# Kernel tuning notes

Hardware: AMD Instinct MI355X
Metric: run time of the kernel (lower is better)

## Reference

```python
import jax, jax.numpy as jnp
import numpy as np

NUM_HEADS = 32
HIDDEN = 4096
ROPE_HID = 2048            # per-head rope dim = 64
Q_LOW = 1536
KV_LOW = 512
B, S = 1, 2048


def _rope(x):
    """Rotate-half RoPE over the last dim of x: [B, S, D]."""
    D = x.shape[-1]
    seq = x.shape[1]
    inv_freq = 1.0 / (10000.0 ** (jnp.arange(0, D, 2, dtype=jnp.float32) / D))  # [D/2]
    ang = jnp.arange(seq, dtype=jnp.float32)[:, None] * inv_freq[None, :]       # [S, D/2]
    cos, sin = jnp.cos(ang), jnp.sin(ang)
    x1, x2 = x[..., : D // 2], x[..., D // 2 :]
    return jnp.concatenate([x1 * cos - x2 * sin, x2 * cos + x1 * sin], axis=-1).astype(x.dtype)


def _rms_norm(x):
    # torch F.rms_norm with no weight; eps defaults to machine epsilon of dtype
    eps = jnp.finfo(x.dtype).eps
    return x * jax.lax.rsqrt(jnp.mean(x * x, axis=-1, keepdims=True) + eps)


def _lin(x, W, b):
    return x @ W.T + b


def setup_inputs() -> dict:
    key = jax.random.key(0)
    ks = jax.random.split(key, 12)
    s = 0.02
    inp = {
        "hidden_state": jax.random.normal(ks[0], (B, S, HIDDEN), jnp.float32),
        "attention_mask": jnp.zeros((B, S, S), jnp.float32),
        "Wq_lr": jax.random.normal(ks[1], (Q_LOW, HIDDEN), jnp.float32) * s,
        "bq_lr": jnp.zeros((Q_LOW,), jnp.float32),
        "Wq_rope": jax.random.normal(ks[2], (ROPE_HID, Q_LOW), jnp.float32) * s,
        "bq_rope": jnp.zeros((ROPE_HID,), jnp.float32),
        "Wq_c": jax.random.normal(ks[3], (HIDDEN, Q_LOW), jnp.float32) * s,
        "bq_c": jnp.zeros((HIDDEN,), jnp.float32),
        "Wkv": jax.random.normal(ks[4], (KV_LOW, HIDDEN), jnp.float32) * s,
        "bkv": jnp.zeros((KV_LOW,), jnp.float32),
        "Wk_rope": jax.random.normal(ks[5], (ROPE_HID // NUM_HEADS, HIDDEN), jnp.float32) * s,
        "bk_rope": jnp.zeros((ROPE_HID // NUM_HEADS,), jnp.float32),
        "Wk_c": jax.random.normal(ks[6], (HIDDEN, KV_LOW), jnp.float32) * s,
        "bk_c": jnp.zeros((HIDDEN,), jnp.float32),
        "Wv": jax.random.normal(ks[7], (HIDDEN, KV_LOW), jnp.float32) * s,
        "bv": jnp.zeros((HIDDEN,), jnp.float32),
        "Wo": jax.random.normal(ks[8], (HIDDEN, HIDDEN), jnp.float32) * s,
        "bo": jnp.zeros((HIDDEN,), jnp.float32),
    }
    return inp


def reference(hidden_state, attention_mask, Wq_lr, bq_lr, Wq_rope, bq_rope, Wq_c, bq_c,
              Wkv, bkv, Wk_rope, bk_rope, Wk_c, bk_c, Wv, bv, Wo, bo):
    H = NUM_HEADS
    b, s, _ = hidden_state.shape
    hd_c = HIDDEN // H        # 128 content head dim
    hd_r = ROPE_HID // H      # 64 rope head dim

    # ---- queries ----
    c_q = _lin(hidden_state, Wq_lr, bq_lr)                       # [B,S,Qlow]
    q_content = _lin(c_q, Wq_c, bq_c).reshape(b, s, H, hd_c)     # [B,S,H,128]
    q_rope = _rope(_lin(c_q, Wq_rope, bq_rope))                  # rope over full 2048 dim
    q_rope = q_rope.reshape(b, s, H, hd_r)                       # [B,S,H,64]
    q = jnp.concatenate([q_content, q_rope], axis=-1)            # [B,S,H,192]

    # ---- keys / values ----
    c_kv = _lin(hidden_state, Wkv, bkv)                          # [B,S,KVlow]
    k_content = _lin(c_kv, Wk_c, bk_c).reshape(b, s, H, hd_c)    # [B,S,H,128]
    k_rope = _rope(_lin(hidden_state, Wk_rope, bk_rope))         # [B,S,64] shared across heads
    k_rope = jnp.broadcast_to(k_rope[:, :, None, :], (b, s, H, hd_r))
    k = jnp.concatenate([k_content, k_rope], axis=-1)            # [B,S,H,192]
    v = _lin(c_kv, Wv, bv).reshape(b, s, H, hd_c)                # [B,S,H,128]

    # ---- qk rms norm (enable_qk_norm=True) ----
    q = _rms_norm(q)
    k = _rms_norm(k)

    # ---- sdpa (bmm + scale + mask + softmax + bmm) ----
    scale = 1.0 / jnp.sqrt(jnp.asarray(q.shape[-1], q.dtype))
    scores = jnp.einsum('bqhd,bkhd->bhqk', q, k) * scale         # [B,H,S,S]
    scores = scores + attention_mask[:, None, :, :]
    attn = jax.nn.softmax(scores, axis=-1)
    out = jnp.einsum('bhqk,bkhd->bqhd', attn, v)                 # [B,S,H,128]
    out = out.reshape(b, s, HIDDEN)
    return _lin(out, Wo, bo)
```

## Files before the change

kernel.cpp:

```cpp
#include <hip/hip_runtime.h>
#include <hip/hip_bf16.h>
#include <math.h>


#define S_LEN 2048
#define HID 4096
#define NH 32
#define HD_C 128
#define HD 192
#define QSTRIDE (NH * HD)

typedef __bf16 bf16x8 __attribute__((ext_vector_type(8)));
typedef float f32x4 __attribute__((ext_vector_type(4)));

__device__ __forceinline__ unsigned short f2bu(float x) {
  __hip_bfloat16 h = __float2bfloat16(x);
  return *reinterpret_cast<unsigned short*>(&h);
}

__global__ __launch_bounds__(256) void f32_to_bf16_vec(
    const float* __restrict__ src, unsigned short* __restrict__ dst, int n8) {
  for (int i = blockIdx.x * 256 + threadIdx.x; i < n8; i += gridDim.x * 256) {
    const float4 a = ((const float4*)src)[(size_t)i * 2];
    const float4 b = ((const float4*)src)[(size_t)i * 2 + 1];
    unsigned short u[8] = {f2bu(a.x), f2bu(a.y), f2bu(a.z), f2bu(a.w),
                           f2bu(b.x), f2bu(b.y), f2bu(b.z), f2bu(b.w)};
    *(float4*)&dst[(size_t)i * 8] = *(float4*)u;
  }
}

__global__ __launch_bounds__(256) void gemm_bf16(
    const unsigned short* __restrict__ A, const unsigned short* __restrict__ W,
    const float* __restrict__ bias, void* __restrict__ Cv,
    int M, int N, int K, int out_mode, int bias_mode) {
  __shared__ __align__(16) unsigned short As[128 * 32];
  __shared__ __align__(16) unsigned short Bs[128 * 32];

  const int tid = threadIdx.x;
  const int wid = tid >> 6, lane = tid & 63;
  const int cl = lane & 15, g = lane >> 4;
  const int wr = wid >> 1, wc = wid & 1;
  const int m0 = blockIdx.y * 128, n0 = blockIdx.x * 128;

  f32x4 acc[4][4] = {};

  for (int k0 = 0; k0 < K; k0 += 32) {
    __syncthreads();
#pragma unroll
    for (int j = 0; j < 2; ++j) {
      const int c = j * 256 + wid * 64 + lane;
      const unsigned short* ga =
          &A[(size_t)(m0 + (c >> 2)) * K + k0 + (c & 3) * 8];
      __builtin_amdgcn_global_load_lds(
          (const __attribute__((address_space(1))) unsigned int*)ga,
          (__attribute__((address_space(3))) unsigned int*)&As[(size_t)(j * 256 + wid * 64) * 8],
          16, 0, 0);
      const unsigned short* gb =
          &W[(size_t)(n0 + (c >> 2)) * K + k0 + (c & 3) * 8];
      __builtin_amdgcn_global_load_lds(
          (const __attribute__((address_space(1))) unsigned int*)gb,
          (__attribute__((address_space(3))) unsigned int*)&Bs[(size_t)(j * 256 + wid * 64) * 8],
          16, 0, 0);
    }
    __syncthreads();

    bf16x8 a[4], b[4];
#pragma unroll
    for (int m = 0; m < 4; ++m)
      a[m] = *(const bf16x8*)&As[(size_t)(wr * 64 + m * 16 + cl) * 32 + g * 8];
#pragma unroll
    for (int n = 0; n < 4; ++n)
      b[n] = *(const bf16x8*)&Bs[(size_t)(wc * 64 + n * 16 + cl) * 32 + g * 8];
#pragma unroll
    for (int m = 0; m < 4; ++m)
#pragma unroll
      for (int n = 0; n < 4; ++n)
        acc[m][n] =
            __builtin_amdgcn_mfma_f32_16x16x32_bf16(a[m], b[n], acc[m][n], 0, 0, 0);
  }

#pragma unroll
  for (int m = 0; m < 4; ++m) {
    const int row = m0 + wr * 64 + m * 16 + g * 4;
#pragma unroll
    for (int n = 0; n < 4; ++n) {
      const int col = n0 + wc * 64 + n * 16 + cl;
#pragma unroll
      for (int r = 0; r < 4; ++r) {
        const float val =
            acc[m][n][r] + (bias_mode ? bias[row + r] : bias[col]);
        if (out_mode == 0)
          ((float*)Cv)[(size_t)(row + r) * N + col] = val;
        else if (out_mode == 1)
          ((__hip_bfloat16*)Cv)[(size_t)(row + r) * QSTRIDE + (col >> 7) * HD +
                                (col & 127)] = __float2bfloat16(val);
        else
          ((__hip_bfloat16*)Cv)[(size_t)(row + r) * N + col] =
              __float2bfloat16(val);
      }
    }
  }
}

template <int TM>
__global__ __launch_bounds__(256) void gemm_bt(
    const float* __restrict__ A, const float* __restrict__ W,
    const float* __restrict__ bias, void* __restrict__ Cv,
    int M, int N, int K, int out_mode) {
  constexpr int RPT = TM / 16;
  __shared__ float As[16][TM + 4];
  __shared__ float Ws[16][68];

  const int tid = threadIdx.x;
  const int tx = tid & 15, ty = tid >> 4;
  const int m0 = blockIdx.y * TM, n0 = blockIdx.x * 64;

  float acc[RPT][4];
#pragma unroll
  for (int i = 0; i < RPT; ++i)
#pragma unroll
    for (int j = 0; j < 4; ++j) acc[i][j] = 0.f;

  for (int k0 = 0; k0 < K; k0 += 16) {
    if (tid < TM * 4) {
      const int r = tid >> 2, c4 = (tid & 3) * 4;
      float4 av = *(const float4*)&A[(size_t)(m0 + r) * K + k0 + c4];
      As[c4 + 0][r] = av.x; As[c4 + 1][r] = av.y;
      As[c4 + 2][r] = av.z; As[c4 + 3][r] = av.w;
    }
    {
      const int r = tid >> 2, c4 = (tid & 3) * 4;
      float4 wv = *(const float4*)&W[(size_t)(n0 + r) * K + k0 + c4];
      Ws[c4 + 0][r] = wv.x; Ws[c4 + 1][r] = wv.y;
      Ws[c4 + 2][r] = wv.z; Ws[c4 + 3][r] = wv.w;
    }
    __syncthreads();
#pragma unroll
    for (int kk = 0; kk < 16; ++kk) {
      const float4 wv = *(const float4*)&Ws[kk][tx * 4];
      const float a = As[kk][ty];
      acc[0][0] += a * wv.x; acc[0][1] += a * wv.y;
      acc[0][2] += a * wv.z; acc[0][3] += a * wv.w;
    }
    __syncthreads();
  }

#pragma unroll
  for (int i = 0; i < RPT; ++i) {
    const int m = m0 + ty * RPT + i;
#pragma unroll
    for (int j = 0; j < 4; ++j) {
      const int n = n0 + tx * 4 + j;
      ((float*)Cv)[(size_t)m * N + n] = acc[i][j] + bias[n];
    }
  }
}

__global__ __launch_bounds__(256) void rope_scatter_q(
    const float* __restrict__ pre, __hip_bfloat16* __restrict__ qh) {
  const int i = blockIdx.x * blockDim.x + threadIdx.x;
  if (i >= S_LEN * 1024) return;
  const int s = i >> 10, p = i & 1023;
  const double invf = pow(10000.0, -((double)(2 * p) / 2048.0));
  double sd, cd;
  sincos((double)s * invf, &sd, &cd);
  const float c = (float)cd, sn = (float)sd;
  const float x1 = pre[(size_t)s * 2048 + p];
  const float x2 = pre[(size_t)s * 2048 + p + 1024];
  const int g1 = p, g2 = p + 1024;
  qh[(size_t)s * QSTRIDE + (g1 >> 6) * HD + 128 + (g1 & 63)] =
      __float2bfloat16(x1 * c - x2 * sn);
  qh[(size_t)s * QSTRIDE + (g2 >> 6) * HD + 128 + (g2 & 63)] =
      __float2bfloat16(x2 * c + x1 * sn);
}

__global__ __launch_bounds__(64) void rope_bcast_k(
    const float* __restrict__ pre, __hip_bfloat16* __restrict__ kh) {
  const int s = blockIdx.x;
  const int j = threadIdx.x;
  const float x = pre[s * 64 + j];
  const float partner = pre[s * 64 + (j ^ 32)];
  const int p = j & 31;
  const double invf = pow(10000.0, -((double)(2 * p) / 64.0));
  double sd, cd;
  sincos((double)s * invf, &sd, &cd);
  const float val = (j < 32) ? x * (float)cd - partner * (float)sd
                             : x * (float)cd + partner * (float)sd;
  const __hip_bfloat16 hv = __float2bfloat16(val);
  for (int h = 0; h < NH; ++h)
    kh[(size_t)s * QSTRIDE + h * HD + 128 + j] = hv;
}

__global__ __launch_bounds__(256) void rmsnorm_rows_bf16(
    __hip_bfloat16* __restrict__ X, int nrows, float scale) {
  const int row = blockIdx.x * 4 + (threadIdx.x >> 6);
  const int lane = threadIdx.x & 63;
  if (row >= nrows) return;
  __hip_bfloat16* p = X + (size_t)row * HD;
  const float v0 = __bfloat162float(p[lane]);
  const float v1 = __bfloat162float(p[lane + 64]);
  const float v2 = __bfloat162float(p[lane + 128]);
  float ss = v0 * v0 + v1 * v1 + v2 * v2;
#pragma unroll
  for (int off = 32; off > 0; off >>= 1) ss += __shfl_xor(ss, off, 64);
  const float r = scale / sqrtf(ss * (1.0f / 192.0f) + 1.1920929e-7f);
  p[lane] = __float2bfloat16(v0 * r);
  p[lane + 64] = __float2bfloat16(v1 * r);
  p[lane + 128] = __float2bfloat16(v2 * r);
}

__global__ __launch_bounds__(256, 2) void flash_attn_mfma2(
    const __hip_bfloat16* __restrict__ Qh, const __hip_bfloat16* __restrict__ Kh,
    const __hip_bfloat16* __restrict__ Vtg, const float* __restrict__ mask,
    __hip_bfloat16* __restrict__ O) {
  __shared__ __align__(16) unsigned short Ks[64][200];
  __shared__ __align__(16) unsigned short Vs[128][72];
  __shared__ __align__(16) unsigned short Ps[4][32][72];

  const int tid = threadIdx.x;
  const int wid = tid >> 6, lane = tid & 63;
  const int cl = lane & 15, g = lane >> 4;
  const int h = blockIdx.y;
  const int Q0 = blockIdx.x * 128 + wid * 32;

  const unsigned short* Q = (const unsigned short*)Qh;
  const unsigned short* K = (const unsigned short*)Kh;
  const unsigned short* Vt = (const unsigned short*)Vtg;

  bf16x8 qreg[2][6];
#pragma unroll
  for (int qt = 0; qt < 2; ++qt)
#pragma unroll
    for (int c = 0; c < 6; ++c)
      qreg[qt][c] = *(const bf16x8*)&Q[(size_t)(Q0 + qt * 16 + cl) * QSTRIDE +
                                       h * HD + c * 32 + g * 8];

  float mprev[2] = {-INFINITY, -INFINITY};
  float lsum[2] = {0.f, 0.f};
  f32x4 acc[2][8] = {};

  for (int k0 = 0; k0 < S_LEN; k0 += 64) {
    __syncthreads();
#pragma unroll
    for (int i = 0; i < 6; ++i) {
      const int c = tid + i * 256;
      const int r = c / 24, cc = c % 24;
      *(float4*)&Ks[r][cc * 8] =
          *(const float4*)&K[(size_t)(k0 + r) * QSTRIDE + h * HD + cc * 8];
    }
#pragma unroll
    for (int i = 0; i < 4; ++i) {
      const int c = tid + i * 256;
      const int d = c >> 3, jc = c & 7;
      *(float4*)&Vs[d][jc * 8] =
          *(const float4*)&Vt[(size_t)(h * HD_C + d) * S_LEN + k0 + jc * 8];
    }
    __syncthreads();

    f32x4 s[2][4] = {};
#pragma unroll
    for (int t = 0; t < 4; ++t) {
#pragma unroll
      for (int c = 0; c < 6; ++c) {
        const bf16x8 kf = *(const bf16x8*)&Ks[t * 16 + cl][c * 32 + g * 8];
        s[0][t] = __builtin_amdgcn_mfma_f32_16x16x32_bf16(kf, qreg[0][c],
                                                          s[0][t], 0, 0, 0);
        s[1][t] = __builtin_amdgcn_mfma_f32_16x16x32_bf16(kf, qreg[1][c],
                                                          s[1][t], 0, 0, 0);
      }
    }
#pragma unroll
    for (int qt = 0; qt < 2; ++qt)
#pragma unroll
      for (int t = 0; t < 4; ++t) {
        const float4 mk = *(const float4*)&mask[(size_t)(Q0 + qt * 16 + cl) *
                                                    S_LEN +
                                                k0 + t * 16 + g * 4];
        s[qt][t][0] += mk.x; s[qt][t][1] += mk.y;
        s[qt][t][2] += mk.z; s[qt][t][3] += mk.w;
      }

#pragma unroll
    for (int qt = 0; qt < 2; ++qt) {
      float mloc = s[qt][0][0];
#pragma unroll
      for (int t = 0; t < 4; ++t)
#pragma unroll
        for (int r = 0; r < 4; ++r) mloc = fmaxf(mloc, s[qt][t][r]);
      mloc = fmaxf(mloc, __shfl_xor(mloc, 16, 64));
      mloc = fmaxf(mloc, __shfl_xor(mloc, 32, 64));
      const float mnew = fmaxf(mprev[qt], mloc);
      const float rsc = __expf(mprev[qt] - mnew);
      mprev[qt] = mnew;
      float p[4][4];
      float ll = 0.f;
#pragma unroll
      for (int t = 0; t < 4; ++t)
#pragma unroll
        for (int r = 0; r < 4; ++r) {
          p[t][r] = __expf(s[qt][t][r] - mnew);
          ll += p[t][r];
        }
      ll += __shfl_xor(ll, 16, 64);
      ll += __shfl_xor(ll, 32, 64);
      lsum[qt] = lsum[qt] * rsc + ll;
#pragma unroll
      for (int dt = 0; dt < 8; ++dt) {
        acc[qt][dt][0] *= rsc; acc[qt][dt][1] *= rsc;
        acc[qt][dt][2] *= rsc; acc[qt][dt][3] *= rsc;
      }
#pragma unroll
      for (int t = 0; t < 4; ++t) {
        unsigned short u[4] = {f2bu(p[t][0]), f2bu(p[t][1]), f2bu(p[t][2]),
                               f2bu(p[t][3])};
        *(double*)&Ps[wid][qt * 16 + cl][t * 16 + g * 4] = *(double*)u;
      }
    }

#pragma unroll
    for (int c = 0; c < 2; ++c) {
      const bf16x8 pf0 = *(const bf16x8*)&Ps[wid][cl][c * 32 + g * 8];
      const bf16x8 pf1 = *(const bf16x8*)&Ps[wid][16 + cl][c * 32 + g * 8];
#pragma unroll
      for (int dt = 0; dt < 8; ++dt) {
        const bf16x8 vf = *(const bf16x8*)&Vs[dt * 16 + cl][c * 32 + g * 8];
        acc[0][dt] = __builtin_amdgcn_mfma_f32_16x16x32_bf16(vf, pf0,
                                                             acc[0][dt], 0, 0, 0);
        acc[1][dt] = __builtin_amdgcn_mfma_f32_16x16x32_bf16(vf, pf1,
                                                             acc[1][dt], 0, 0, 0);
      }
    }
  }

#pragma unroll
  for (int qt = 0; qt < 2; ++qt) {
    const float il = 1.0f / lsum[qt];
    const size_t base = (size_t)(Q0 + qt * 16 + cl) * HID + h * HD_C;
#pragma unroll
    for (int dt = 0; dt < 8; ++dt) {
      unsigned short u[4] = {
          f2bu(acc[qt][dt][0] * il), f2bu(acc[qt][dt][1] * il),
          f2bu(acc[qt][dt][2] * il), f2bu(acc[qt][dt][3] * il)};
      *(double*)&((unsigned short*)O)[base + dt * 16 + g * 4] = *(double*)u;
    }
  }
}

extern "C" void kernel_launch(void* const* d_in, const int* in_sizes, int n_in,
                              void* d_out, int out_size, void* d_ws,
                              size_t ws_size, hipStream_t stream) {
  const float* X       = (const float*)d_in[0];
  const float* mask    = (const float*)d_in[1];
  const float* Wq_lr   = (const float*)d_in[2];
  const float* bq_lr   = (const float*)d_in[3];
  const float* Wq_rope = (const float*)d_in[4];
  const float* bq_rope = (const float*)d_in[5];
  const float* Wq_c    = (const float*)d_in[6];
  const float* bq_c    = (const float*)d_in[7];
  const float* Wkv     = (const float*)d_in[8];
  const float* bkv     = (const float*)d_in[9];
  const float* Wk_rope = (const float*)d_in[10];
  const float* bk_rope = (const float*)d_in[11];
  const float* Wk_c    = (const float*)d_in[12];
  const float* bk_c    = (const float*)d_in[13];
  const float* Wv      = (const float*)d_in[14];
  const float* bv      = (const float*)d_in[15];
  const float* Wo      = (const float*)d_in[16];
  const float* bo      = (const float*)d_in[17];
  float* out = (float*)d_out;

  char* w = (char*)d_ws;
  unsigned short* Xb   = (unsigned short*)w;  w += (size_t)2048 * 4096 * 2;
  unsigned short* wbuf = (unsigned short*)w;  w += (size_t)4096 * 4096 * 2;
  unsigned short* c_qb = (unsigned short*)w;  w += (size_t)2048 * 1536 * 2;
  unsigned short* c_kvb= (unsigned short*)w;  w += (size_t)2048 * 512 * 2;
  float* fb            = (float*)w;           w += (size_t)2048 * 2048 * 4;
  __hip_bfloat16* qh   = (__hip_bfloat16*)w;  w += (size_t)2048 * 6144 * 2;
  __hip_bfloat16* kh   = (__hip_bfloat16*)w;  w += (size_t)2048 * 6144 * 2;
  __hip_bfloat16* vt   = (__hip_bfloat16*)w;  w += (size_t)4096 * 2048 * 2;
  __hip_bfloat16* ob   = (__hip_bfloat16*)fb;

  const dim3 blk(256);
  auto cvt = [&](const float* s, unsigned short* d, int n) {
    const int n8 = n / 8;
    const int nb = min(2048, (n8 + 255) / 256);
    f32_to_bf16_vec<<<nb, blk, 0, stream>>>(s, d, n8);
  };

  cvt(X, Xb, 2048 * 4096);
  cvt(Wq_lr, wbuf, 1536 * 4096);
  gemm_bf16<<<dim3(12, 16), blk, 0, stream>>>(Xb, wbuf, bq_lr, c_qb,
                                              2048, 1536, 4096, 2, 0);
  cvt(Wq_c, wbuf, 4096 * 1536);
  gemm_bf16<<<dim3(32, 16), blk, 0, stream>>>(c_qb, wbuf, bq_c, qh,
                                              2048, 4096, 1536, 1, 0);
  cvt(Wq_rope, wbuf, 2048 * 1536);
  gemm_bf16<<<dim3(16, 16), blk, 0, stream>>>(c_qb, wbuf, bq_rope, fb,
                                              2048, 2048, 1536, 0, 0);
  rope_scatter_q<<<(S_LEN * 1024) / 256, blk, 0, stream>>>(fb, qh);
  cvt(Wkv, wbuf, 512 * 4096);
  gemm_bf16<<<dim3(4, 16), blk, 0, stream>>>(Xb, wbuf, bkv, c_kvb,
                                             2048, 512, 4096, 2, 0);
  cvt(Wk_c, wbuf, 4096 * 512);
  gemm_bf16<<<dim3(32, 16), blk, 0, stream>>>(c_kvb, wbuf, bk_c, kh,
                                              2048, 4096, 512, 1, 0);
  gemm_bt<16><<<dim3(1, 128), blk, 0, stream>>>(X, Wk_rope, bk_rope, fb,
                                                2048, 64, 4096, 0);
  rope_bcast_k<<<S_LEN, dim3(64), 0, stream>>>(fb, kh);
  cvt(Wv, wbuf, 4096 * 512);
  gemm_bf16<<<dim3(16, 32), blk, 0, stream>>>(wbuf, c_kvb, bv, vt,
                                              4096, 2048, 512, 2, 1);
  rmsnorm_rows_bf16<<<(S_LEN * NH) / 4, blk, 0, stream>>>(
      qh, S_LEN * NH, 0.07216878364870322f);
  rmsnorm_rows_bf16<<<(S_LEN * NH) / 4, blk, 0, stream>>>(kh, S_LEN * NH, 1.0f);
  flash_attn_mfma2<<<dim3(S_LEN / 128, NH), blk, 0, stream>>>(qh, kh, vt, mask,
                                                              ob);
  cvt(Wo, wbuf, 4096 * 4096);
  gemm_bf16<<<dim3(32, 16), blk, 0, stream>>>((const unsigned short*)ob, wbuf,
                                              bo, out, 2048, 4096, 4096, 0, 0);
}
```

Measured before the change: 1.062 ms.

## Fuse weight bf16 conversion into GEMM loads and merge KV/rope-K projections

The GEMM kernel is templated to read fp32 operands directly and convert them to bf16 while staging into shared memory, removing the separate weight conversion kernels and their global round trips. The Wkv and Wk_rope projections are concatenated into one padded weight matrix so the K rope projection runs on the MFMA GEMM instead of a scalar fp32 kernel. RoPE angle computation moves from double to float precision. The trade-off is that fp32 tiles are loaded synchronously through registers rather than via direct global-to-LDS loads, doubling bytes fetched per tile, and float trig may slightly change accuracy at large positions.

```diff
diff --git a/kernel.cpp b/kernel.cpp
--- a/kernel.cpp
+++ b/kernel.cpp
@@ -29,10 +29,33 @@
   }
 }
 
-__global__ __launch_bounds__(256) void gemm_bf16(
-    const unsigned short* __restrict__ A, const unsigned short* __restrict__ W,
+__global__ __launch_bounds__(256) void assemble_wkv(
+    const float* __restrict__ Wkv, const float* __restrict__ bkv,
+    const float* __restrict__ Wk_rope, const float* __restrict__ bk_rope,
+    float* __restrict__ Wdst, float* __restrict__ bdst) {
+  const int i = blockIdx.x * 256 + threadIdx.x;
+  const int row = i >> 10, c4 = i & 1023;
+  float4 v = {0.f, 0.f, 0.f, 0.f};
+  if (row < 512)
+    v = ((const float4*)Wkv)[(size_t)row * 1024 + c4];
+  else if (row < 576)
+    v = ((const float4*)Wk_rope)[(size_t)(row - 512) * 1024 + c4];
+  ((float4*)Wdst)[i] = v;
+  if (blockIdx.x == 0 && threadIdx.x < 160) {
+#pragma unroll
+    for (int t = 0; t < 4; ++t) {
+      const int b = threadIdx.x * 4 + t;
+      bdst[b] = b < 512 ? bkv[b] : (b < 576 ? bk_rope[b - 512] : 0.f);
+    }
+  }
+}
+
+template <int AF32, int BF32>
+__global__ __launch_bounds__(256) void gemm_mfma(
+    const void* __restrict__ Av, const void* __restrict__ Wv_,
     const float* __restrict__ bias, void* __restrict__ Cv,
-    int M, int N, int K, int out_mode, int bias_mode) {
+    int M, int N, int K, int out_mode, int bias_mode,
+    float* __restrict__ aux) {
   __shared__ __align__(16) unsigned short As[128 * 32];
   __shared__ __align__(16) unsigned short Bs[128 * 32];
 
@@ -46,21 +69,55 @@
 
   for (int k0 = 0; k0 < K; k0 += 32) {
     __syncthreads();
-#pragma unroll
-    for (int j = 0; j < 2; ++j) {
-      const int c = j * 256 + wid * 64 + lane;
-      const unsigned short* ga =
-          &A[(size_t)(m0 + (c >> 2)) * K + k0 + (c & 3) * 8];
-      __builtin_amdgcn_global_load_lds(
-          (const __attribute__((address_space(1))) unsigned int*)ga,
-          (__attribute__((address_space(3))) unsigned int*)&As[(size_t)(j * 256 + wid * 64) * 8],
-          16, 0, 0);
-      const unsigned short* gb =
-          &W[(size_t)(n0 + (c >> 2)) * K + k0 + (c & 3) * 8];
-      __builtin_amdgcn_global_load_lds(
-          (const __attribute__((address_space(1))) unsigned int*)gb,
-          (__attribute__((address_space(3))) unsigned int*)&Bs[(size_t)(j * 256 + wid * 64) * 8],
-          16, 0, 0);
+    if constexpr (AF32) {
+      const float* Af = (const float*)Av;
+#pragma unroll
+      for (int j = 0; j < 2; ++j) {
+        const int c = j * 256 + tid;
+        const float* gs = &Af[(size_t)(m0 + (c >> 2)) * K + k0 + (c & 3) * 8];
+        const float4 f0 = *(const float4*)gs;
+        const float4 f1 = *(const float4*)(gs + 4);
+        unsigned short u[8] = {f2bu(f0.x), f2bu(f0.y), f2bu(f0.z), f2bu(f0.w),
+                               f2bu(f1.x), f2bu(f1.y), f2bu(f1.z), f2bu(f1.w)};
+        *(float4*)&As[(size_t)c * 8] = *(float4*)u;
+      }
+    } else {
+      const unsigned short* Ab = (const unsigned short*)Av;
+#pragma unroll
+      for (int j = 0; j < 2; ++j) {
+        const int c = j * 256 + wid * 64 + lane;
+        const unsigned short* ga =
+            &Ab[(size_t)(m0 + (c >> 2)) * K + k0 + (c & 3) * 8];
+        __builtin_amdgcn_global_load_lds(
+            (const __attribute__((address_space(1))) unsigned int*)ga,
+            (__attribute__((address_space(3))) unsigned int*)&As[(size_t)(j * 256 + wid * 64) * 8],
+            16, 0, 0);
+      }
+    }
+    if constexpr (BF32) {
+      const float* Wf = (const float*)Wv_;
+#pragma unroll
+      for (int j = 0; j < 2; ++j) {
+        const int c = j * 256 + tid;
+        const float* gs = &Wf[(size_t)(n0 + (c >> 2)) * K + k0 + (c & 3) * 8];
+        const float4 f0 = *(const float4*)gs;
+        const float4 f1 = *(const float4*)(gs + 4);
+        unsigned short u[8] = {f2bu(f0.x), f2bu(f0.y), f2bu(f0.z), f2bu(f0.w),
+                               f2bu(f1.x), f2bu(f1.y), f2bu(f1.z), f2bu(f1.w)};
+        *(float4*)&Bs[(size_t)c * 8] = *(float4*)u;
+      }
+    } else {
+      const unsigned short* Wb = (const unsigned short*)Wv_;
+#pragma unroll
+      for (int j = 0; j < 2; ++j) {
+        const int c = j * 256 + wid * 64 + lane;
+        const unsigned short* gb =
+            &Wb[(size_t)(n0 + (c >> 2)) * K + k0 + (c & 3) * 8];
+        __builtin_amdgcn_global_load_lds(
+            (const __attribute__((address_space(1))) unsigned int*)gb,
+            (__attribute__((address_space(3))) unsigned int*)&Bs[(size_t)(j * 256 + wid * 64) * 8],
+            16, 0, 0);
+      }
     }
     __syncthreads();
 
@@ -94,64 +151,17 @@
         else if (out_mode == 1)
           ((__hip_bfloat16*)Cv)[(size_t)(row + r) * QSTRIDE + (col >> 7) * HD +
                                 (col & 127)] = __float2bfloat16(val);
-        else
+        else if (out_mode == 2)
           ((__hip_bfloat16*)Cv)[(size_t)(row + r) * N + col] =
               __float2bfloat16(val);
-      }
-    }
-  }
-}
-
-template <int TM>
-__global__ __launch_bounds__(256) void gemm_bt(
-    const float* __restrict__ A, const float* __restrict__ W,
-    const float* __restrict__ bias, void* __restrict__ Cv,
-    int M, int N, int K, int out_mode) {
-  constexpr int RPT = TM / 16;
-  __shared__ float As[16][TM + 4];
-  __shared__ float Ws[16][68];
-
-  const int tid = threadIdx.x;
-  const int tx = tid & 15, ty = tid >> 4;
-  const int m0 = blockIdx.y * TM, n0 = blockIdx.x * 64;
-
-  float acc[RPT][4];
-#pragma unroll
-  for (int i = 0; i < RPT; ++i)
-#pragma unroll
-    for (int j = 0; j < 4; ++j) acc[i][j] = 0.f;
-
-  for (int k0 = 0; k0 < K; k0 += 16) {
-    if (tid < TM * 4) {
-      const int r = tid >> 2, c4 = (tid & 3) * 4;
-      float4 av = *(const float4*)&A[(size_t)(m0 + r) * K + k0 + c4];
-      As[c4 + 0][r] = av.x; As[c4 + 1][r] = av.y;
-      As[c4 + 2][r] = av.z; As[c4 + 3][r] = av.w;
-    }
-    {
-      const int r = tid >> 2, c4 = (tid & 3) * 4;
-      float4 wv = *(const float4*)&W[(size_t)(n0 + r) * K + k0 + c4];
-      Ws[c4 + 0][r] = wv.x; Ws[c4 + 1][r] = wv.y;
-      Ws[c4 + 2][r] = wv.z; Ws[c4 + 3][r] = wv.w;
-    }
-    __syncthreads();
-#pragma unroll
-    for (int kk = 0; kk < 16; ++kk) {
-      const float4 wv = *(const float4*)&Ws[kk][tx * 4];
-      const float a = As[kk][ty];
-      acc[0][0] += a * wv.x; acc[0][1] += a * wv.y;
-      acc[0][2] += a * wv.z; acc[0][3] += a * wv.w;
-    }
-    __syncthreads();
-  }
-
-#pragma unroll
-  for (int i = 0; i < RPT; ++i) {
-    const int m = m0 + ty * RPT + i;
-#pragma unroll
-    for (int j = 0; j < 4; ++j) {
-      const int n = n0 + tx * 4 + j;
-      ((float*)Cv)[(size_t)m * N + n] = acc[i][j] + bias[n];
+        else {
+          if (col < 512)
+            ((__hip_bfloat16*)Cv)[(size_t)(row + r) * 512 + col] =
+                __float2bfloat16(val);
+          else if (col < 576)
+            aux[(size_t)(row + r) * 64 + (col - 512)] = val;
+        }
+      }
     }
   }
 }
@@ -161,17 +171,16 @@
   const int i = blockIdx.x * blockDim.x + threadIdx.x;
   if (i >= S_LEN * 1024) return;
   const int s = i >> 10, p = i & 1023;
-  const double invf = pow(10000.0, -((double)(2 * p) / 2048.0));
-  double sd, cd;
-  sincos((double)s * invf, &sd, &cd);
-  const float c = (float)cd, sn = (float)sd;
+  const float invf = powf(10000.0f, -((float)(2 * p) / 2048.0f));
+  float sn, cs;
+  sincosf((float)s * invf, &sn, &cs);
   const float x1 = pre[(size_t)s * 2048 + p];
   const float x2 = pre[(size_t)s * 2048 + p + 1024];
   const int g1 = p, g2 = p + 1024;
   qh[(size_t)s * QSTRIDE + (g1 >> 6) * HD + 128 + (g1 & 63)] =
-      __float2bfloat16(x1 * c - x2 * sn);
+      __float2bfloat16(x1 * cs - x2 * sn);
   qh[(size_t)s * QSTRIDE + (g2 >> 6) * HD + 128 + (g2 & 63)] =
-      __float2bfloat16(x2 * c + x1 * sn);
+      __float2bfloat16(x2 * cs + x1 * sn);
 }
 
 __global__ __launch_bounds__(64) void rope_bcast_k(
@@ -181,11 +190,10 @@
   const float x = pre[s * 64 + j];
   const float partner = pre[s * 64 + (j ^ 32)];
   const int p = j & 31;
-  const double invf = pow(10000.0, -((double)(2 * p) / 64.0));
-  double sd, cd;
-  sincos((double)s * invf, &sd, &cd);
-  const float val = (j < 32) ? x * (float)cd - partner * (float)sd
-                             : x * (float)cd + partner * (float)sd;
+  const float invf = powf(10000.0f, -((float)(2 * p) / 64.0f));
+  float sn, cs;
+  sincosf((float)s * invf, &sn, &cs);
+  const float val = (j < 32) ? x * cs - partner * sn : x * cs + partner * sn;
   const __hip_bfloat16 hv = __float2bfloat16(val);
   for (int h = 0; h < NH; ++h)
     kh[(size_t)s * QSTRIDE + h * HD + 128 + j] = hv;
@@ -371,51 +379,41 @@
 
   char* w = (char*)d_ws;
   unsigned short* Xb   = (unsigned short*)w;  w += (size_t)2048 * 4096 * 2;
-  unsigned short* wbuf = (unsigned short*)w;  w += (size_t)4096 * 4096 * 2;
+  float* wkvf          = (float*)w;           w += (size_t)640 * 4096 * 4;
+  float* bkvf          = (float*)w;           w += 4096;
   unsigned short* c_qb = (unsigned short*)w;  w += (size_t)2048 * 1536 * 2;
   unsigned short* c_kvb= (unsigned short*)w;  w += (size_t)2048 * 512 * 2;
   float* fb            = (float*)w;           w += (size_t)2048 * 2048 * 4;
+  float* fbk           = (float*)w;           w += (size_t)2048 * 64 * 4;
   __hip_bfloat16* qh   = (__hip_bfloat16*)w;  w += (size_t)2048 * 6144 * 2;
   __hip_bfloat16* kh   = (__hip_bfloat16*)w;  w += (size_t)2048 * 6144 * 2;
   __hip_bfloat16* vt   = (__hip_bfloat16*)w;  w += (size_t)4096 * 2048 * 2;
   __hip_bfloat16* ob   = (__hip_bfloat16*)fb;
 
   const dim3 blk(256);
-  auto cvt = [&](const float* s, unsigned short* d, int n) {
-    const int n8 = n / 8;
-    const int nb = min(2048, (n8 + 255) / 256);
-    f32_to_bf16_vec<<<nb, blk, 0, stream>>>(s, d, n8);
-  };
-
-  cvt(X, Xb, 2048 * 4096);
-  cvt(Wq_lr, wbuf, 1536 * 4096);
-  gemm_bf16<<<dim3(12, 16), blk, 0, stream>>>(Xb, wbuf, bq_lr, c_qb,
-                                              2048, 1536, 4096, 2, 0);
-  cvt(Wq_c, wbuf, 4096 * 1536);
-  gemm_bf16<<<dim3(32, 16), blk, 0, stream>>>(c_qb, wbuf, bq_c, qh,
-                                              2048, 4096, 1536, 1, 0);
-  cvt(Wq_rope, wbuf, 2048 * 1536);
-  gemm_bf16<<<dim3(16, 16), blk, 0, stream>>>(c_qb, wbuf, bq_rope, fb,
-                                              2048, 2048, 1536, 0, 0);
+
+  f32_to_bf16_vec<<<2048, blk, 0, stream>>>(X, Xb, 2048 * 4096 / 8);
+  assemble_wkv<<<2560, blk, 0, stream>>>(Wkv, bkv, Wk_rope, bk_rope, wkvf,
+                                         bkvf);
+  gemm_mfma<0, 1><<<dim3(12, 16), blk, 0, stream>>>(
+      Xb, Wq_lr, bq_lr, c_qb, 2048, 1536, 4096, 2, 0, nullptr);
+  gemm_mfma<0, 1><<<dim3(32, 16), blk, 0, stream>>>(
+      c_qb, Wq_c, bq_c, qh, 2048, 4096, 1536, 1, 0, nullptr);
+  gemm_mfma<0, 1><<<dim3(16, 16), blk, 0, stream>>>(
+      c_qb, Wq_rope, bq_rope, fb, 2048, 2048, 1536, 0, 0, nullptr);
   rope_scatter_q<<<(S_LEN * 1024) / 256, blk, 0, stream>>>(fb, qh);
-  cvt(Wkv, wbuf, 512 * 4096);
-  gemm_bf16<<<dim3(4, 16), blk, 0, stream>>>(Xb, wbuf, bkv, c_kvb,
-                                             2048, 512, 4096, 2, 0);
-  cvt(Wk_c, wbuf, 4096 * 512);
-  gemm_bf16<<<dim3(32, 16), blk, 0, stream>>>(c_kvb, wbuf, bk_c, kh,
-                                              2048, 4096, 512, 1, 0);
-  gemm_bt<16><<<dim3(1, 128), blk, 0, stream>>>(X, Wk_rope, bk_rope, fb,
-                                                2048, 64, 4096, 0);
-  rope_bcast_k<<<S_LEN, dim3(64), 0, stream>>>(fb, kh);
-  cvt(Wv, wbuf, 4096 * 512);
-  gemm_bf16<<<dim3(16, 32), blk, 0, stream>>>(wbuf, c_kvb, bv, vt,
-                                              4096, 2048, 512, 2, 1);
+  gemm_mfma<0, 1><<<dim3(5, 16), blk, 0, stream>>>(
+      Xb, wkvf, bkvf, c_kvb, 2048, 640, 4096, 3, 0, fbk);
+  rope_bcast_k<<<S_LEN, dim3(64), 0, stream>>>(fbk, kh);
+  gemm_mfma<0, 1><<<dim3(32, 16), blk, 0, stream>>>(
+      c_kvb, Wk_c, bk_c, kh, 2048, 4096, 512, 1, 0, nullptr);
+  gemm_mfma<1, 0><<<dim3(16, 32), blk, 0, stream>>>(
+      Wv, c_kvb, bv, vt, 4096, 2048, 512, 2, 1, nullptr);
   rmsnorm_rows_bf16<<<(S_LEN * NH) / 4, blk, 0, stream>>>(
       qh, S_LEN * NH, 0.07216878364870322f);
   rmsnorm_rows_bf16<<<(S_LEN * NH) / 4, blk, 0, stream>>>(kh, S_LEN * NH, 1.0f);
   flash_attn_mfma2<<<dim3(S_LEN / 128, NH), blk, 0, stream>>>(qh, kh, vt, mask,
                                                               ob);
-  cvt(Wo, wbuf, 4096 * 4096);
-  gemm_bf16<<<dim3(32, 16), blk, 0, stream>>>((const unsigned short*)ob, wbuf,
-                                              bo, out, 2048, 4096, 4096, 0, 0);
-}
+  gemm_mfma<0, 1><<<dim3(32, 16), blk, 0, stream>>>(
+      (const unsigned short*)ob, Wo, bo, out, 2048, 4096, 4096, 0, 0, nullptr);
+}
```

Result: faster. 993.9 us (-6.4%).
